# Performance work log

Hardware: AMD Instinct MI355X
Metric: run time of the kernel (lower is better)

The kernel has to match this reference:

```python
import jax, jax.numpy as jnp
import numpy as np

EPS = 1e-8  # torch cosine_similarity eps

def _cnorm(x):
    return jnp.maximum(jnp.linalg.norm(x, axis=-1), EPS)

def setup_inputs() -> dict:
    key = jax.random.key(0)
    ks = jax.random.split(key, 9)
    B, K, dp, Ms = 16384, 16, 64, 32
    content = jax.random.normal(ks[0], (B, K, dp), jnp.float32)
    types = jax.random.uniform(ks[1], (B, K, 3), jnp.float32)
    conf = jax.random.uniform(ks[2], (B, K), jnp.float32)
    S = jax.random.normal(ks[3], (B, Ms, dp), jnp.float32)
    s1 = 1.0 / np.sqrt(dp)   # torch Linear init bound, fan_in=dp
    s2 = 1.0 / np.sqrt(2 * dp)  # fan_in=2*dp
    W_ante = jax.random.uniform(ks[4], (dp, dp), jnp.float32, -s1, s1)
    W_cons = jax.random.uniform(ks[5], (dp, 2 * dp), jnp.float32, -s2, s2)
    W_gamma_w = jax.random.uniform(ks[6], (dp, 2 * dp), jnp.float32, -s2, s2)
    W_gamma_b = jnp.zeros((dp,), jnp.float32)
    log_fire_threshold = jnp.asarray(np.log(0.5), jnp.float32)
    return {"content": content, "types": types, "conf": conf, "S": S,
            "W_ante": W_ante, "W_cons": W_cons, "W_gamma_w": W_gamma_w,
            "W_gamma_b": W_gamma_b, "log_fire_threshold": log_fire_threshold}

def reference(content, types, conf, S, W_ante, W_cons, W_gamma_w, W_gamma_b, log_fire_threshold):
    # InferenceEngine.forward_chain, vectorized over rules and batch.
    B, K, dp = content.shape
    p_fact = types[..., 0]  # FACT channel
    p_rule = types[..., 1]  # RULE channel
    thr = jnp.exp(log_fire_threshold)

    ante = content @ W_ante.T                                   # [B,K,dp]
    dots = jnp.einsum('bkd,bjd->bkj', ante, content)            # [B,K_rule,K_fact]
    sim = dots / (_cnorm(ante)[:, :, None] * _cnorm(content)[:, None, :])
    match_scores = sim * p_fact[:, None, :]
    match_strength = jnp.einsum('bkj,bj->bk', match_scores, conf)
    fire = jax.nn.sigmoid((match_strength - thr) / 0.5) * p_rule  # [B,K]
    matched = jnp.einsum('bkj,bjd->bkd', match_scores, content)
    new_fact = jnp.concatenate([content, matched], -1) @ W_cons.T  # [B,K,dp]
    derived_conf = fire * conf                                     # [B,K]

    def soft_write(S, cand, dconf):
        # batched LatentScratchpad.soft_write; cand [B,dp], dconf [B]
        dot = jnp.einsum('bd,bmd->bm', cand, S)
        s = dot / (_cnorm(cand)[:, None] * _cnorm(S))
        alpha = jax.nn.softmax(s * 4.0, axis=-1)                  # [B,Ms]
        best = jnp.argmax(alpha, axis=-1)
        best_slots = jnp.take_along_axis(S, best[:, None, None], axis=1)[:, 0, :]
        gamma = jax.nn.sigmoid(jnp.concatenate([best_slots, cand], -1) @ W_gamma_w.T + W_gamma_b)
        new_content = gamma * cand + (1.0 - gamma) * best_slots
        return S + dconf[:, None, None] * alpha[..., None] * (new_content[:, None, :] - S)

    def step(S, xs):
        nf_k, fire_k, dc_k = xs
        S_w = soft_write(S, nf_k, dc_k)
        mask = (fire_k > 0.1)[:, None, None]  # replaces per-element .item() branch
        return jnp.where(mask, S_w, S), None

    xs = (jnp.swapaxes(new_fact, 0, 1), fire.T, derived_conf.T)   # scan over K rules (sequential dep on S)
    S_new, _ = jax.lax.scan(step, S, xs)
    best_derived_conf = jnp.max(derived_conf, axis=-1)
    return S_new, best_derived_conf
```

## Files before the change

### kernel.cpp

```cpp
#include <hip/hip_runtime.h>
#include <math.h>

typedef float v2f __attribute__((ext_vector_type(2)));
typedef float v4f __attribute__((ext_vector_type(4)));
typedef short bs8 __attribute__((ext_vector_type(8)));
typedef int   i4  __attribute__((ext_vector_type(4)));

__device__ __forceinline__ float hsum(v2f a) { return a.x + a.y; }
__device__ __forceinline__ float rsq_(float x) { return __builtin_amdgcn_rsqf(fmaxf(x, 1e-16f)); }
__device__ __forceinline__ float rcp_(float x) { return __builtin_amdgcn_rcpf(x); }

__device__ __forceinline__ void pk4(v2f& acc, v4f a, v4f b) {
    acc += a.xy * b.xy;
    acc += a.zw * b.zw;
}

__device__ __forceinline__ short bf16rne_(float x) {
    unsigned u = __float_as_uint(x);
    return (short)((u + 0x7FFFu + ((u >> 16) & 1)) >> 16);
}
__device__ __forceinline__ float bf2f_(short s) {
    return __uint_as_float((unsigned)(unsigned short)s << 16);
}
__device__ __forceinline__ int cvtpk_(float lo, float hi) {
    int r;
    asm("v_cvt_pk_bf16_f32 %0, %1, %2" : "=v"(r) : "v"(lo), "v"(hi));
    return r;
}
__device__ __forceinline__ float xsum32_(float x) {
    auto r = __builtin_amdgcn_permlane32_swap(__float_as_int(x), __float_as_int(x), false, false);
    return __int_as_float(r[0]) + __int_as_float(r[1]);
}

template<int CTRL>
__device__ __forceinline__ float dpp_add_(float x) {
    int r = __builtin_amdgcn_update_dpp(0, __float_as_int(x), CTRL, 0xF, 0xF, true);
    return x + __int_as_float(r);
}
template<int CTRL>
__device__ __forceinline__ float dpp_max_(float x) {
    int r = __builtin_amdgcn_update_dpp(__float_as_int(x), __float_as_int(x), CTRL, 0xF, 0xF, false);
    return fmaxf(x, __int_as_float(r));
}
__device__ __forceinline__ float dpp_sum32h(float x) {
    x = dpp_add_<0x111>(x);
    x = dpp_add_<0x112>(x);
    x = dpp_add_<0x114>(x);
    x = dpp_add_<0x118>(x);
    x = dpp_add_<0x142>(x);
    return __int_as_float(__builtin_amdgcn_readlane(__float_as_int(x), 31));
}
__device__ __forceinline__ float dpp_max32h(float x) {
    x = dpp_max_<0x111>(x);
    x = dpp_max_<0x112>(x);
    x = dpp_max_<0x114>(x);
    x = dpp_max_<0x118>(x);
    x = dpp_max_<0x142>(x);
    return __int_as_float(__builtin_amdgcn_readlane(__float_as_int(x), 31));
}

__global__ __launch_bounds__(256, 2)
void dense_kernel(const float* __restrict__ content,
                  const float* __restrict__ types,
                  const float* __restrict__ conf,
                  const float* __restrict__ W_ante,
                  const float* __restrict__ W_cons,
                  const float* __restrict__ W_gw,
                  const float* __restrict__ lft,
                  float* __restrict__ out, int B)
{
    const int tid = threadIdx.x;
    const int l = tid & 63;
    const int w = tid >> 6;
    const int b = blockIdx.x * 4 + w;

    __shared__ float s_cont[4][16*68];
    __shared__ float s_scr [4][16*68];
    __shared__ float s_ms  [4][16*20];
    __shared__ float s_sm  [4][96];
    __shared__ bs8   s_bA[512];
    __shared__ bs8   s_b1[512];
    __shared__ bs8   s_b2[512];
    __shared__ bs8   s_bG[512];

    #pragma unroll
    for (int it = 0; it < 8; it++) {
        const int fid = tid + it*256;
        const int mat = fid >> 9, rem = fid & 511;
        const int fl  = rem & 63;
        const int row = ((rem >> 7) & 3)*16 + (fl & 15);
        const int kb  = ((rem >> 6) & 1)*32 + (fl >> 4)*8;
        const float* src = (mat == 0) ? (W_ante + row*64 + kb)
                         : (mat == 1) ? (W_cons + row*128 + kb)
                         : (mat == 2) ? (W_cons + row*128 + 64 + kb)
                         :              (W_gw  + row*128 + 64 + kb);
        bs8 v;
        #pragma unroll
        for (int e = 0; e < 8; e++) v[e] = bf16rne_(src[e]);
        bs8* dst = (mat == 0) ? s_bA : (mat == 1) ? s_b1 : (mat == 2) ? s_b2 : s_bG;
        dst[rem] = v;
    }
    __syncthreads();
    if (b >= B) return;

    float* cont = s_cont[w];
    float* scr  = s_scr[w];
    float* ms   = s_ms[w];
    float* sm   = s_sm[w];

    const float thr = expf(lft[0]);

    float c[16];
    const float* cb = content + ((size_t)b << 10);
    #pragma unroll
    for (int k = 0; k < 16; k++) {
        float v = cb[(k << 6) + l];
        c[k] = v;
        cont[k*68 + l] = v;
    }
    if (l < 16) {
        sm[0  + l] = conf[((size_t)b << 4) + l];
        sm[16 + l] = types[(((size_t)b << 4) + l)*3 + 0];
        sm[32 + l] = types[(((size_t)b << 4) + l)*3 + 1];
    }

    {
        const int k = l & 15, q = l >> 4;
        const v4f* row = (const v4f*)&cont[k*68 + q*16];
        v2f s2 = {0.f, 0.f};
        #pragma unroll
        for (int i = 0; i < 4; i++) { v4f v = row[i]; pk4(s2, v, v); }
        float s = hsum(s2);
        s += __shfl_xor(s, 16, 64);
        s += __shfl_xor(s, 32, 64);
        if (l < 16) sm[48 + l] = rsq_(s);
    }

    bs8 aC[2];
    #pragma unroll
    for (int s = 0; s < 2; s++) {
        const float* ap = &cont[(l & 15)*68 + s*32 + (l >> 4)*8];
        v4f p0 = *(const v4f*)ap;
        v4f p1 = *(const v4f*)(ap + 4);
        bs8 v;
        v[0]=bf16rne_(p0.x); v[1]=bf16rne_(p0.y); v[2]=bf16rne_(p0.z); v[3]=bf16rne_(p0.w);
        v[4]=bf16rne_(p1.x); v[5]=bf16rne_(p1.y); v[6]=bf16rne_(p1.z); v[7]=bf16rne_(p1.w);
        aC[s] = v;
    }

    #pragma unroll
    for (int t = 0; t < 4; t++) {
        v4f acc = {0.f, 0.f, 0.f, 0.f};
        acc = __builtin_amdgcn_mfma_f32_16x16x32_bf16(aC[0], s_bA[(t*2+0)*64 + l], acc, 0, 0, 0);
        acc = __builtin_amdgcn_mfma_f32_16x16x32_bf16(aC[1], s_bA[(t*2+1)*64 + l], acc, 0, 0, 0);
        #pragma unroll
        for (int r = 0; r < 4; r++)
            scr[((l >> 4)*4 + r)*68 + t*16 + (l & 15)] = acc[r];
    }

    {
        const int k = l & 15, q = l >> 4;
        const v4f* row = (const v4f*)&scr[k*68 + q*16];
        v2f s2 = {0.f, 0.f};
        #pragma unroll
        for (int i = 0; i < 4; i++) { v4f v = row[i]; pk4(s2, v, v); }
        float s = hsum(s2);
        s += __shfl_xor(s, 16, 64);
        s += __shfl_xor(s, 32, 64);
        if (l < 16) sm[64 + l] = rsq_(s);
    }

    {
        const int k = l & 15, jg4 = (l >> 4) * 4;
        const v4f* ar = (const v4f*)&scr[k*68];
        const v4f* c0 = (const v4f*)&cont[(jg4+0)*68];
        const v4f* c1 = (const v4f*)&cont[(jg4+1)*68];
        const v4f* c2 = (const v4f*)&cont[(jg4+2)*68];
        const v4f* c3 = (const v4f*)&cont[(jg4+3)*68];
        v2f d0 = {0,0}, d1 = {0,0}, d2 = {0,0}, d3 = {0,0};
        #pragma unroll
        for (int i = 0; i < 16; i++) {
            v4f a = ar[i];
            v4f x0 = c0[i]; d0 += a.xy*x0.xy; d0 += a.zw*x0.zw;
            v4f x1 = c1[i]; d1 += a.xy*x1.xy; d1 += a.zw*x1.zw;
            v4f x2 = c2[i]; d2 += a.xy*x2.xy; d2 += a.zw*x2.zw;
            v4f x3 = c3[i]; d3 += a.xy*x3.xy; d3 += a.zw*x3.zw;
        }
        const float ra = sm[64 + k];
        v4f res;
        res.x = hsum(d0) * ra * sm[48 + jg4+0] * sm[16 + jg4+0];
        res.y = hsum(d1) * ra * sm[48 + jg4+1] * sm[16 + jg4+1];
        res.z = hsum(d2) * ra * sm[48 + jg4+2] * sm[16 + jg4+2];
        res.w = hsum(d3) * ra * sm[48 + jg4+3] * sm[16 + jg4+3];
        *(v4f*)&ms[k*20 + jg4] = res;
    }

    float dc_l = 0.f;
    if (l < 16) {
        const v4f* mr = (const v4f*)&ms[l*20];
        const v4f* cf = (const v4f*)&sm[0];
        v2f st = {0.f, 0.f};
        #pragma unroll
        for (int i = 0; i < 4; i++) { v4f m4 = mr[i]; v4f f4 = cf[i]; st += m4.xy*f4.xy; st += m4.zw*f4.zw; }
        float str = hsum(st);
        float fire = sm[32 + l] * rcp_(1.0f + __expf(-(str - thr) * 2.0f));
        float dcf  = fire * sm[0 + l];
        out[((size_t)b << 11) + 1024 + l] = fire;
        out[((size_t)b << 11) + 1040 + l] = dcf;
        dc_l = dcf;
    }
    {
        float mv = dc_l;
        mv = fmaxf(mv, __shfl_xor(mv, 1, 64));
        mv = fmaxf(mv, __shfl_xor(mv, 2, 64));
        mv = fmaxf(mv, __shfl_xor(mv, 4, 64));
        mv = fmaxf(mv, __shfl_xor(mv, 8, 64));
        if (l == 0) out[((size_t)B << 11) + b] = mv;
    }

    float mt[16];
    #pragma unroll
    for (int k = 0; k < 16; k++) {
        const v4f* mr = (const v4f*)&ms[k*20];
        v2f m2 = {0.f, 0.f};
        #pragma unroll
        for (int i = 0; i < 4; i++) {
            v4f m4 = mr[i];
            v2f clo = {c[4*i+0], c[4*i+1]};
            v2f chi = {c[4*i+2], c[4*i+3]};
            m2 += m4.xy*clo; m2 += m4.zw*chi;
        }
        mt[k] = hsum(m2);
    }
    #pragma unroll
    for (int k = 0; k < 16; k++) scr[k*68 + l] = mt[k];

    bs8 aM[2];
    #pragma unroll
    for (int s = 0; s < 2; s++) {
        const float* ap = &scr[(l & 15)*68 + s*32 + (l >> 4)*8];
        v4f p0 = *(const v4f*)ap;
        v4f p1 = *(const v4f*)(ap + 4);
        bs8 v;
        v[0]=bf16rne_(p0.x); v[1]=bf16rne_(p0.y); v[2]=bf16rne_(p0.z); v[3]=bf16rne_(p0.w);
        v[4]=bf16rne_(p1.x); v[5]=bf16rne_(p1.y); v[6]=bf16rne_(p1.z); v[7]=bf16rne_(p1.w);
        aM[s] = v;
    }

    v4f nfacc[4];
    #pragma unroll
    for (int t = 0; t < 4; t++) {
        v4f acc = {0.f, 0.f, 0.f, 0.f};
        acc = __builtin_amdgcn_mfma_f32_16x16x32_bf16(aC[0], s_b1[(t*2+0)*64 + l], acc, 0, 0, 0);
        acc = __builtin_amdgcn_mfma_f32_16x16x32_bf16(aC[1], s_b1[(t*2+1)*64 + l], acc, 0, 0, 0);
        acc = __builtin_amdgcn_mfma_f32_16x16x32_bf16(aM[0], s_b2[(t*2+0)*64 + l], acc, 0, 0, 0);
        acc = __builtin_amdgcn_mfma_f32_16x16x32_bf16(aM[1], s_b2[(t*2+1)*64 + l], acc, 0, 0, 0);
        nfacc[t] = acc;
    }

    #pragma unroll
    for (int t = 0; t < 4; t++) {
        #pragma unroll
        for (int r = 0; r < 4; r++) {
            const int krow = (l >> 4)*4 + r, dcol = t*16 + (l & 15);
            scr[krow*68 + dcol] = nfacc[t][r];
            out[((size_t)b << 11) + (size_t)(krow << 6) + dcol] = nfacc[t][r];
        }
    }

    #pragma unroll
    for (int r = 0; r < 4; r++) {
        float s = 0.f;
        #pragma unroll
        for (int t = 0; t < 4; t++) s += nfacc[t][r]*nfacc[t][r];
        s += __shfl_xor(s, 1, 64);
        s += __shfl_xor(s, 2, 64);
        s += __shfl_xor(s, 4, 64);
        s += __shfl_xor(s, 8, 64);
        if ((l & 15) == 0)
            out[((size_t)b << 11) + 1056 + (l >> 4)*4 + r] = rsq_(s);
    }

    bs8 aN[2];
    #pragma unroll
    for (int s = 0; s < 2; s++) {
        const float* ap = &scr[(l & 15)*68 + s*32 + (l >> 4)*8];
        v4f p0 = *(const v4f*)ap;
        v4f p1 = *(const v4f*)(ap + 4);
        bs8 v;
        v[0]=bf16rne_(p0.x); v[1]=bf16rne_(p0.y); v[2]=bf16rne_(p0.z); v[3]=bf16rne_(p0.w);
        v[4]=bf16rne_(p1.x); v[5]=bf16rne_(p1.y); v[6]=bf16rne_(p1.z); v[7]=bf16rne_(p1.w);
        aN[s] = v;
    }

    unsigned short* gco = (unsigned short*)(out + ((size_t)b << 11) + 1088);
    #pragma unroll
    for (int t = 0; t < 4; t++) {
        v4f acc = {0.f, 0.f, 0.f, 0.f};
        acc = __builtin_amdgcn_mfma_f32_16x16x32_bf16(aN[0], s_bG[(t*2+0)*64 + l], acc, 0, 0, 0);
        acc = __builtin_amdgcn_mfma_f32_16x16x32_bf16(aN[1], s_bG[(t*2+1)*64 + l], acc, 0, 0, 0);
        #pragma unroll
        for (int r = 0; r < 4; r++)
            gco[(((l >> 4)*4 + r) << 6) + t*16 + (l & 15)] = (unsigned short)bf16rne_(acc[r]);
    }
}

__global__ __launch_bounds__(512, 4)
void scan_kernel(const float* __restrict__ Sg,
                 const float* __restrict__ W_gw,
                 const float* __restrict__ W_gb,
                 float* __restrict__ out, int B)
{
    const int t = threadIdx.x;
    const int l = t & 63;
    const int w = t >> 6;
    const int b = (blockIdx.x << 3) + w;

    __shared__ bs8   bG2[512];
    __shared__ float snf_  [8][16*64];
    __shared__ float smeta_[8][48];
    __shared__ float bsb_  [8][68];
    float* snf   = snf_[w];
    float* smeta = smeta_[w];
    float* bsb   = bsb_[w];

    const int m = l & 31, h = l >> 5;

    {
        const int rem = t;
        const int fl  = rem & 63;
        const int row = ((rem >> 7) & 3)*16 + (fl & 15);
        const int kb  = ((rem >> 6) & 1)*32 + (fl >> 4)*8;
        const float* src = W_gw + (size_t)row*128 + kb;
        bs8 v;
        #pragma unroll
        for (int e = 0; e < 8; e++) v[e] = bf16rne_(src[e]);
        bG2[rem] = v;
    }

    v2f Sreg[16];

    if (b < B) {
        if (l < 48) smeta[l] = out[((size_t)b << 11) + 1024 + l];

        const float* nfb = out + ((size_t)b << 11);
        #pragma unroll
        for (int i = 0; i < 4; i++) {
            *(v4f*)&snf[i*256 + l*4] = *(const v4f*)&nfb[i*256 + l*4];
        }

        const float* srow = Sg + ((size_t)b << 11) + (m << 6) + (h << 5);
        #pragma unroll
        for (int i = 0; i < 8; i++) {
            v4f v = *(const v4f*)&srow[i*4];
            Sreg[2*i]   = v.xy;
            Sreg[2*i+1] = v.zw;
        }
    }

    __syncthreads();
    if (b >= B) return;

    const unsigned short* gcg = (const unsigned short*)(out + ((size_t)b << 11) + 1088);
    const float gb = W_gb[l];
    const int q = l >> 4;

    #pragma unroll 1
    for (int k = 0; k < 16; k++) {
        const float fire = smeta[k];
        if (fire <= 0.1f) continue;
        const float dck  = smeta[16 + k];
        const float rncn = smeta[32 + k];
        const unsigned short gcu = gcg[(k << 6) + l];
        const float cd   = snf[(k << 6) + l];

        v2f d2 = {0.f, 0.f}, n2 = {0.f, 0.f};
        {
            const v4f* cr = (const v4f*)&snf[(k << 6) + (h << 5)];
            #pragma unroll
            for (int i = 0; i < 8; i++) {
                v4f c = cr[i];
                d2 += Sreg[2*i]*c.xy;       d2 += Sreg[2*i+1]*c.zw;
                n2 += Sreg[2*i]*Sreg[2*i];  n2 += Sreg[2*i+1]*Sreg[2*i+1];
            }
        }
        const float dt = xsum32_(hsum(d2));
        const float nn = xsum32_(hsum(n2));
        const float sc = dt * rsq_(nn) * rncn;
        const float e  = __expf(4.0f * sc);

        const float mx = dpp_max32h(sc);
        const unsigned long long bal = __ballot(sc == mx);
        const int best = __ffsll(bal & 0xffffffffULL) - 1;

        if (m == best) {
            #pragma unroll
            for (int j = 0; j < 8; j++) {
                v4f v = { Sreg[2*j].x, Sreg[2*j].y, Sreg[2*j+1].x, Sreg[2*j+1].y };
                *(v4f*)&bsb[(h << 5) + j*4] = v;
            }
        }

        const float tot = dpp_sum32h(e);
        const float wm  = dck * e * rcp_(tot);

        bs8 af[2];
        #pragma unroll
        for (int s = 0; s < 2; s++) {
            const float* bp = &bsb[s*32 + q*8];
            v4f p0 = *(const v4f*)bp;
            v4f p1 = *(const v4f*)(bp + 4);
            i4 pk;
            pk[0] = cvtpk_(p0.x, p0.y);
            pk[1] = cvtpk_(p0.z, p0.w);
            pk[2] = cvtpk_(p1.x, p1.y);
            pk[3] = cvtpk_(p1.z, p1.w);
            af[s] = __builtin_bit_cast(bs8, pk);
        }
        __builtin_amdgcn_s_setprio(1);
        v4f g0 = {0,0,0,0}, g1 = {0,0,0,0}, g2a = {0,0,0,0}, g3 = {0,0,0,0};
        g0 = __builtin_amdgcn_mfma_f32_16x16x32_bf16(af[0], bG2[0*64 + l], g0, 0, 0, 0);
        g1 = __builtin_amdgcn_mfma_f32_16x16x32_bf16(af[0], bG2[2*64 + l], g1, 0, 0, 0);
        g2a = __builtin_amdgcn_mfma_f32_16x16x32_bf16(af[0], bG2[4*64 + l], g2a, 0, 0, 0);
        g3 = __builtin_amdgcn_mfma_f32_16x16x32_bf16(af[0], bG2[6*64 + l], g3, 0, 0, 0);
        g0 = __builtin_amdgcn_mfma_f32_16x16x32_bf16(af[1], bG2[1*64 + l], g0, 0, 0, 0);
        g1 = __builtin_amdgcn_mfma_f32_16x16x32_bf16(af[1], bG2[3*64 + l], g1, 0, 0, 0);
        g2a = __builtin_amdgcn_mfma_f32_16x16x32_bf16(af[1], bG2[5*64 + l], g2a, 0, 0, 0);
        g3 = __builtin_amdgcn_mfma_f32_16x16x32_bf16(af[1], bG2[7*64 + l], g3, 0, 0, 0);
        __builtin_amdgcn_s_setprio(0);
        const float gdot = (q < 2) ? ((q == 0) ? g0[0] : g1[0])
                                   : ((q == 2) ? g2a[0] : g3[0]);

        const float gck = bf2f_((short)gcu);
        const float g = gb + gck + gdot;
        const float gamma = rcp_(1.0f + __expf(-g));
        const float bsd = bsb[l];
        bsb[l] = gamma*cd + (1.0f - gamma)*bsd;

        const v2f wm2 = {wm, wm};
        {
            const v4f* nr = (const v4f*)&bsb[h << 5];
            #pragma unroll
            for (int i = 0; i < 8; i++) {
                v4f nc = nr[i];
                Sreg[2*i]   += wm2 * (nc.xy - Sreg[2*i]);
                Sreg[2*i+1] += wm2 * (nc.zw - Sreg[2*i+1]);
            }
        }
    }

    {
        float* ob = out + ((size_t)b << 11) + (m << 6) + (h << 5);
        #pragma unroll
        for (int j = 0; j < 8; j++) {
            v4f v = { Sreg[2*j].x, Sreg[2*j].y, Sreg[2*j+1].x, Sreg[2*j+1].y };
            *(v4f*)&ob[j*4] = v;
        }
    }
}

extern "C" void kernel_launch(void* const* d_in, const int* in_sizes, int n_in,
                              void* d_out, int out_size, void* d_ws, size_t ws_size,
                              hipStream_t stream) {
    const float* content = (const float*)d_in[0];
    const float* types   = (const float*)d_in[1];
    const float* conf    = (const float*)d_in[2];
    const float* S       = (const float*)d_in[3];
    const float* W_ante  = (const float*)d_in[4];
    const float* W_cons  = (const float*)d_in[5];
    const float* W_gw    = (const float*)d_in[6];
    const float* W_gb    = (const float*)d_in[7];
    const float* lft     = (const float*)d_in[8];

    const int B = in_sizes[0] / 1024;

    hipLaunchKernelGGL(dense_kernel, dim3((B + 3) / 4), dim3(256), 0, stream,
                       content, types, conf, W_ante, W_cons, W_gw, lft, (float*)d_out, B);
    hipLaunchKernelGGL(scan_kernel, dim3((B + 7) / 8), dim3(512), 0, stream,
                       S, W_gw, W_gb, (float*)d_out, B);
}
```

Measured before the change: 199.2 us.

## Fuse dense and scan kernels, keeping intermediates in shared memory

```diff
diff --git a/kernel.cpp b/kernel.cpp
--- a/kernel.cpp
+++ b/kernel.cpp
@@ -22,8 +22,8 @@
 __device__ __forceinline__ float bf2f_(short s) {
     return __uint_as_float((unsigned)(unsigned short)s << 16);
 }
-__device__ __forceinline__ int cvtpk_(float lo, float hi) {
-    int r;
+__device__ __forceinline__ unsigned cvtpk_(float lo, float hi) {
+    unsigned r;
     asm("v_cvt_pk_bf16_f32 %0, %1, %2" : "=v"(r) : "v"(lo), "v"(hi));
     return r;
 }
@@ -60,12 +60,14 @@
 }
 
 __global__ __launch_bounds__(256, 2)
-void dense_kernel(const float* __restrict__ content,
+void fused_kernel(const float* __restrict__ content,
                   const float* __restrict__ types,
                   const float* __restrict__ conf,
+                  const float* __restrict__ Sg,
                   const float* __restrict__ W_ante,
                   const float* __restrict__ W_cons,
                   const float* __restrict__ W_gw,
+                  const float* __restrict__ W_gb,
                   const float* __restrict__ lft,
                   float* __restrict__ out, int B)
 {
@@ -73,6 +75,7 @@
     const int l = tid & 63;
     const int w = tid >> 6;
     const int b = blockIdx.x * 4 + w;
+    const bool act = (b < B);
 
     __shared__ float s_cont[4][16*68];
     __shared__ float s_scr [4][16*68];
@@ -82,6 +85,14 @@
     __shared__ bs8   s_b1[512];
     __shared__ bs8   s_b2[512];
     __shared__ bs8   s_bG[512];
+
+    float* cont = s_cont[w];
+    float* scr  = s_scr[w];
+    float* ms   = s_ms[w];
+    float* sm   = s_sm[w];
+    unsigned short* gcB = (unsigned short*)cont;
+    float* smeta = cont + 512;
+    float* bsb   = cont + 560;
 
     #pragma unroll
     for (int it = 0; it < 8; it++) {
@@ -101,233 +112,217 @@
         dst[rem] = v;
     }
     __syncthreads();
-    if (b >= B) return;
-
-    float* cont = s_cont[w];
-    float* scr  = s_scr[w];
-    float* ms   = s_ms[w];
-    float* sm   = s_sm[w];
 
     const float thr = expf(lft[0]);
 
-    float c[16];
-    const float* cb = content + ((size_t)b << 10);
+    if (act) {
+        float c[16];
+        const float* cb = content + ((size_t)b << 10);
+        #pragma unroll
+        for (int k = 0; k < 16; k++) {
+            float v = cb[(k << 6) + l];
+            c[k] = v;
+            cont[k*68 + l] = v;
+        }
+        if (l < 16) {
+            sm[0  + l] = conf[((size_t)b << 4) + l];
+            sm[16 + l] = types[(((size_t)b << 4) + l)*3 + 0];
+            sm[32 + l] = types[(((size_t)b << 4) + l)*3 + 1];
+        }
+
+        {
+            const int k = l & 15, q = l >> 4;
+            const v4f* row = (const v4f*)&cont[k*68 + q*16];
+            v2f s2 = {0.f, 0.f};
+            #pragma unroll
+            for (int i = 0; i < 4; i++) { v4f v = row[i]; pk4(s2, v, v); }
+            float s = hsum(s2);
+            s += __shfl_xor(s, 16, 64);
+            s += __shfl_xor(s, 32, 64);
+            if (l < 16) sm[48 + l] = rsq_(s);
+        }
+
+        bs8 aC[2];
+        #pragma unroll
+        for (int s = 0; s < 2; s++) {
+            const float* ap = &cont[(l & 15)*68 + s*32 + (l >> 4)*8];
+            v4f p0 = *(const v4f*)ap;
+            v4f p1 = *(const v4f*)(ap + 4);
+            bs8 v;
+            v[0]=bf16rne_(p0.x); v[1]=bf16rne_(p0.y); v[2]=bf16rne_(p0.z); v[3]=bf16rne_(p0.w);
+            v[4]=bf16rne_(p1.x); v[5]=bf16rne_(p1.y); v[6]=bf16rne_(p1.z); v[7]=bf16rne_(p1.w);
+            aC[s] = v;
+        }
+
+        #pragma unroll
+        for (int t = 0; t < 4; t++) {
+            v4f acc = {0.f, 0.f, 0.f, 0.f};
+            acc = __builtin_amdgcn_mfma_f32_16x16x32_bf16(aC[0], s_bA[(t*2+0)*64 + l], acc, 0, 0, 0);
+            acc = __builtin_amdgcn_mfma_f32_16x16x32_bf16(aC[1], s_bA[(t*2+1)*64 + l], acc, 0, 0, 0);
+            #pragma unroll
+            for (int r = 0; r < 4; r++)
+                scr[((l >> 4)*4 + r)*68 + t*16 + (l & 15)] = acc[r];
+        }
+
+        {
+            const int k = l & 15, q = l >> 4;
+            const v4f* row = (const v4f*)&scr[k*68 + q*16];
+            v2f s2 = {0.f, 0.f};
+            #pragma unroll
+            for (int i = 0; i < 4; i++) { v4f v = row[i]; pk4(s2, v, v); }
+            float s = hsum(s2);
+            s += __shfl_xor(s, 16, 64);
+            s += __shfl_xor(s, 32, 64);
+            if (l < 16) sm[64 + l] = rsq_(s);
+        }
+
+        {
+            const int k = l & 15, jg4 = (l >> 4) * 4;
+            const v4f* ar = (const v4f*)&scr[k*68];
+            const v4f* c0 = (const v4f*)&cont[(jg4+0)*68];
+            const v4f* c1 = (const v4f*)&cont[(jg4+1)*68];
+            const v4f* c2 = (const v4f*)&cont[(jg4+2)*68];
+            const v4f* c3 = (const v4f*)&cont[(jg4+3)*68];
+            v2f d0 = {0,0}, d1 = {0,0}, d2 = {0,0}, d3 = {0,0};
+            #pragma unroll
+            for (int i = 0; i < 16; i++) {
+                v4f a = ar[i];
+                v4f x0 = c0[i]; d0 += a.xy*x0.xy; d0 += a.zw*x0.zw;
+                v4f x1 = c1[i]; d1 += a.xy*x1.xy; d1 += a.zw*x1.zw;
+                v4f x2 = c2[i]; d2 += a.xy*x2.xy; d2 += a.zw*x2.zw;
+                v4f x3 = c3[i]; d3 += a.xy*x3.xy; d3 += a.zw*x3.zw;
+            }
+            const float ra = sm[64 + k];
+            v4f res;
+            res.x = hsum(d0) * ra * sm[48 + jg4+0] * sm[16 + jg4+0];
+            res.y = hsum(d1) * ra * sm[48 + jg4+1] * sm[16 + jg4+1];
+            res.z = hsum(d2) * ra * sm[48 + jg4+2] * sm[16 + jg4+2];
+            res.w = hsum(d3) * ra * sm[48 + jg4+3] * sm[16 + jg4+3];
+            *(v4f*)&ms[k*20 + jg4] = res;
+        }
+
+        float dc_l = 0.f;
+        if (l < 16) {
+            const v4f* mr = (const v4f*)&ms[l*20];
+            const v4f* cf = (const v4f*)&sm[0];
+            v2f st = {0.f, 0.f};
+            #pragma unroll
+            for (int i = 0; i < 4; i++) { v4f m4 = mr[i]; v4f f4 = cf[i]; st += m4.xy*f4.xy; st += m4.zw*f4.zw; }
+            float str = hsum(st);
+            float fire = sm[32 + l] * rcp_(1.0f + __expf(-(str - thr) * 2.0f));
+            float dcf  = fire * sm[0 + l];
+            smeta[l]      = fire;
+            smeta[16 + l] = dcf;
+            dc_l = dcf;
+        }
+        {
+            float mv = dc_l;
+            mv = fmaxf(mv, __shfl_xor(mv, 1, 64));
+            mv = fmaxf(mv, __shfl_xor(mv, 2, 64));
+            mv = fmaxf(mv, __shfl_xor(mv, 4, 64));
+            mv = fmaxf(mv, __shfl_xor(mv, 8, 64));
+            if (l == 0) out[((size_t)B << 11) + b] = mv;
+        }
+
+        float mt[16];
+        #pragma unroll
+        for (int k = 0; k < 16; k++) {
+            const v4f* mr = (const v4f*)&ms[k*20];
+            v2f m2 = {0.f, 0.f};
+            #pragma unroll
+            for (int i = 0; i < 4; i++) {
+                v4f m4 = mr[i];
+                v2f clo = {c[4*i+0], c[4*i+1]};
+                v2f chi = {c[4*i+2], c[4*i+3]};
+                m2 += m4.xy*clo; m2 += m4.zw*chi;
+            }
+            mt[k] = hsum(m2);
+        }
+        #pragma unroll
+        for (int k = 0; k < 16; k++) scr[k*68 + l] = mt[k];
+
+        bs8 aM[2];
+        #pragma unroll
+        for (int s = 0; s < 2; s++) {
+            const float* ap = &scr[(l & 15)*68 + s*32 + (l >> 4)*8];
+            v4f p0 = *(const v4f*)ap;
+            v4f p1 = *(const v4f*)(ap + 4);
+            bs8 v;
+            v[0]=bf16rne_(p0.x); v[1]=bf16rne_(p0.y); v[2]=bf16rne_(p0.z); v[3]=bf16rne_(p0.w);
+            v[4]=bf16rne_(p1.x); v[5]=bf16rne_(p1.y); v[6]=bf16rne_(p1.z); v[7]=bf16rne_(p1.w);
+            aM[s] = v;
+        }
+
+        v4f nfacc[4];
+        #pragma unroll
+        for (int t = 0; t < 4; t++) {
+            v4f acc = {0.f, 0.f, 0.f, 0.f};
+            acc = __builtin_amdgcn_mfma_f32_16x16x32_bf16(aC[0], s_b1[(t*2+0)*64 + l], acc, 0, 0, 0);
+            acc = __builtin_amdgcn_mfma_f32_16x16x32_bf16(aC[1], s_b1[(t*2+1)*64 + l], acc, 0, 0, 0);
+            acc = __builtin_amdgcn_mfma_f32_16x16x32_bf16(aM[0], s_b2[(t*2+0)*64 + l], acc, 0, 0, 0);
+            acc = __builtin_amdgcn_mfma_f32_16x16x32_bf16(aM[1], s_b2[(t*2+1)*64 + l], acc, 0, 0, 0);
+            nfacc[t] = acc;
+        }
+
+        #pragma unroll
+        for (int t = 0; t < 4; t++) {
+            #pragma unroll
+            for (int r = 0; r < 4; r++)
+                scr[((l >> 4)*4 + r)*68 + t*16 + (l & 15)] = nfacc[t][r];
+        }
+
+        #pragma unroll
+        for (int r = 0; r < 4; r++) {
+            float s = 0.f;
+            #pragma unroll
+            for (int t = 0; t < 4; t++) s += nfacc[t][r]*nfacc[t][r];
+            s += __shfl_xor(s, 1, 64);
+            s += __shfl_xor(s, 2, 64);
+            s += __shfl_xor(s, 4, 64);
+            s += __shfl_xor(s, 8, 64);
+            if ((l & 15) == 0)
+                smeta[32 + (l >> 4)*4 + r] = rsq_(s);
+        }
+
+        bs8 aN[2];
+        #pragma unroll
+        for (int s = 0; s < 2; s++) {
+            const float* ap = &scr[(l & 15)*68 + s*32 + (l >> 4)*8];
+            v4f p0 = *(const v4f*)ap;
+            v4f p1 = *(const v4f*)(ap + 4);
+            bs8 v;
+            v[0]=bf16rne_(p0.x); v[1]=bf16rne_(p0.y); v[2]=bf16rne_(p0.z); v[3]=bf16rne_(p0.w);
+            v[4]=bf16rne_(p1.x); v[5]=bf16rne_(p1.y); v[6]=bf16rne_(p1.z); v[7]=bf16rne_(p1.w);
+            aN[s] = v;
+        }
+
+        #pragma unroll
+        for (int t = 0; t < 4; t++) {
+            v4f acc = {0.f, 0.f, 0.f, 0.f};
+            acc = __builtin_amdgcn_mfma_f32_16x16x32_bf16(aN[0], s_bG[(t*2+0)*64 + l], acc, 0, 0, 0);
+            acc = __builtin_amdgcn_mfma_f32_16x16x32_bf16(aN[1], s_bG[(t*2+1)*64 + l], acc, 0, 0, 0);
+            #pragma unroll
+            for (int r = 0; r < 4; r++)
+                gcB[(((l >> 4)*4 + r) << 6) + t*16 + (l & 15)] = (unsigned short)bf16rne_(acc[r]);
+        }
+    }
+
+    const int m = l & 31, h = l >> 5;
+    v2f Sreg[16];
+    if (act) {
+        const float* srow = Sg + ((size_t)b << 11) + (m << 6) + (h << 5);
+        #pragma unroll
+        for (int i = 0; i < 8; i++) {
+            v4f v = *(const v4f*)&srow[i*4];
+            Sreg[2*i]   = v.xy;
+            Sreg[2*i+1] = v.zw;
+        }
+    }
+
+    __syncthreads();
     #pragma unroll
-    for (int k = 0; k < 16; k++) {
-        float v = cb[(k << 6) + l];
-        c[k] = v;
-        cont[k*68 + l] = v;
-    }
-    if (l < 16) {
-        sm[0  + l] = conf[((size_t)b << 4) + l];
-        sm[16 + l] = types[(((size_t)b << 4) + l)*3 + 0];
-        sm[32 + l] = types[(((size_t)b << 4) + l)*3 + 1];
-    }
-
-    {
-        const int k = l & 15, q = l >> 4;
-        const v4f* row = (const v4f*)&cont[k*68 + q*16];
-        v2f s2 = {0.f, 0.f};
-        #pragma unroll
-        for (int i = 0; i < 4; i++) { v4f v = row[i]; pk4(s2, v, v); }
-        float s = hsum(s2);
-        s += __shfl_xor(s, 16, 64);
-        s += __shfl_xor(s, 32, 64);
-        if (l < 16) sm[48 + l] = rsq_(s);
-    }
-
-    bs8 aC[2];
-    #pragma unroll
-    for (int s = 0; s < 2; s++) {
-        const float* ap = &cont[(l & 15)*68 + s*32 + (l >> 4)*8];
-        v4f p0 = *(const v4f*)ap;
-        v4f p1 = *(const v4f*)(ap + 4);
-        bs8 v;
-        v[0]=bf16rne_(p0.x); v[1]=bf16rne_(p0.y); v[2]=bf16rne_(p0.z); v[3]=bf16rne_(p0.w);
-        v[4]=bf16rne_(p1.x); v[5]=bf16rne_(p1.y); v[6]=bf16rne_(p1.z); v[7]=bf16rne_(p1.w);
-        aC[s] = v;
-    }
-
-    #pragma unroll
-    for (int t = 0; t < 4; t++) {
-        v4f acc = {0.f, 0.f, 0.f, 0.f};
-        acc = __builtin_amdgcn_mfma_f32_16x16x32_bf16(aC[0], s_bA[(t*2+0)*64 + l], acc, 0, 0, 0);
-        acc = __builtin_amdgcn_mfma_f32_16x16x32_bf16(aC[1], s_bA[(t*2+1)*64 + l], acc, 0, 0, 0);
-        #pragma unroll
-        for (int r = 0; r < 4; r++)
-            scr[((l >> 4)*4 + r)*68 + t*16 + (l & 15)] = acc[r];
-    }
-
-    {
-        const int k = l & 15, q = l >> 4;
-        const v4f* row = (const v4f*)&scr[k*68 + q*16];
-        v2f s2 = {0.f, 0.f};
-        #pragma unroll
-        for (int i = 0; i < 4; i++) { v4f v = row[i]; pk4(s2, v, v); }
-        float s = hsum(s2);
-        s += __shfl_xor(s, 16, 64);
-        s += __shfl_xor(s, 32, 64);
-        if (l < 16) sm[64 + l] = rsq_(s);
-    }
-
-    {
-        const int k = l & 15, jg4 = (l >> 4) * 4;
-        const v4f* ar = (const v4f*)&scr[k*68];
-        const v4f* c0 = (const v4f*)&cont[(jg4+0)*68];
-        const v4f* c1 = (const v4f*)&cont[(jg4+1)*68];
-        const v4f* c2 = (const v4f*)&cont[(jg4+2)*68];
-        const v4f* c3 = (const v4f*)&cont[(jg4+3)*68];
-        v2f d0 = {0,0}, d1 = {0,0}, d2 = {0,0}, d3 = {0,0};
-        #pragma unroll
-        for (int i = 0; i < 16; i++) {
-            v4f a = ar[i];
-            v4f x0 = c0[i]; d0 += a.xy*x0.xy; d0 += a.zw*x0.zw;
-            v4f x1 = c1[i]; d1 += a.xy*x1.xy; d1 += a.zw*x1.zw;
-            v4f x2 = c2[i]; d2 += a.xy*x2.xy; d2 += a.zw*x2.zw;
-            v4f x3 = c3[i]; d3 += a.xy*x3.xy; d3 += a.zw*x3.zw;
-        }
-        const float ra = sm[64 + k];
-        v4f res;
-        res.x = hsum(d0) * ra * sm[48 + jg4+0] * sm[16 + jg4+0];
-        res.y = hsum(d1) * ra * sm[48 + jg4+1] * sm[16 + jg4+1];
-        res.z = hsum(d2) * ra * sm[48 + jg4+2] * sm[16 + jg4+2];
-        res.w = hsum(d3) * ra * sm[48 + jg4+3] * sm[16 + jg4+3];
-        *(v4f*)&ms[k*20 + jg4] = res;
-    }
-
-    float dc_l = 0.f;
-    if (l < 16) {
-        const v4f* mr = (const v4f*)&ms[l*20];
-        const v4f* cf = (const v4f*)&sm[0];
-        v2f st = {0.f, 0.f};
-        #pragma unroll
-        for (int i = 0; i < 4; i++) { v4f m4 = mr[i]; v4f f4 = cf[i]; st += m4.xy*f4.xy; st += m4.zw*f4.zw; }
-        float str = hsum(st);
-        float fire = sm[32 + l] * rcp_(1.0f + __expf(-(str - thr) * 2.0f));
-        float dcf  = fire * sm[0 + l];
-        out[((size_t)b << 11) + 1024 + l] = fire;
-        out[((size_t)b << 11) + 1040 + l] = dcf;
-        dc_l = dcf;
-    }
-    {
-        float mv = dc_l;
-        mv = fmaxf(mv, __shfl_xor(mv, 1, 64));
-        mv = fmaxf(mv, __shfl_xor(mv, 2, 64));
-        mv = fmaxf(mv, __shfl_xor(mv, 4, 64));
-        mv = fmaxf(mv, __shfl_xor(mv, 8, 64));
-        if (l == 0) out[((size_t)B << 11) + b] = mv;
-    }
-
-    float mt[16];
-    #pragma unroll
-    for (int k = 0; k < 16; k++) {
-        const v4f* mr = (const v4f*)&ms[k*20];
-        v2f m2 = {0.f, 0.f};
-        #pragma unroll
-        for (int i = 0; i < 4; i++) {
-            v4f m4 = mr[i];
-            v2f clo = {c[4*i+0], c[4*i+1]};
-            v2f chi = {c[4*i+2], c[4*i+3]};
-            m2 += m4.xy*clo; m2 += m4.zw*chi;
-        }
-        mt[k] = hsum(m2);
-    }
-    #pragma unroll
-    for (int k = 0; k < 16; k++) scr[k*68 + l] = mt[k];
-
-    bs8 aM[2];
-    #pragma unroll
-    for (int s = 0; s < 2; s++) {
-        const float* ap = &scr[(l & 15)*68 + s*32 + (l >> 4)*8];
-        v4f p0 = *(const v4f*)ap;
-        v4f p1 = *(const v4f*)(ap + 4);
-        bs8 v;
-        v[0]=bf16rne_(p0.x); v[1]=bf16rne_(p0.y); v[2]=bf16rne_(p0.z); v[3]=bf16rne_(p0.w);
-        v[4]=bf16rne_(p1.x); v[5]=bf16rne_(p1.y); v[6]=bf16rne_(p1.z); v[7]=bf16rne_(p1.w);
-        aM[s] = v;
-    }
-
-    v4f nfacc[4];
-    #pragma unroll
-    for (int t = 0; t < 4; t++) {
-        v4f acc = {0.f, 0.f, 0.f, 0.f};
-        acc = __builtin_amdgcn_mfma_f32_16x16x32_bf16(aC[0], s_b1[(t*2+0)*64 + l], acc, 0, 0, 0);
-        acc = __builtin_amdgcn_mfma_f32_16x16x32_bf16(aC[1], s_b1[(t*2+1)*64 + l], acc, 0, 0, 0);
-        acc = __builtin_amdgcn_mfma_f32_16x16x32_bf16(aM[0], s_b2[(t*2+0)*64 + l], acc, 0, 0, 0);
-        acc = __builtin_amdgcn_mfma_f32_16x16x32_bf16(aM[1], s_b2[(t*2+1)*64 + l], acc, 0, 0, 0);
-        nfacc[t] = acc;
-    }
-
-    #pragma unroll
-    for (int t = 0; t < 4; t++) {
-        #pragma unroll
-        for (int r = 0; r < 4; r++) {
-            const int krow = (l >> 4)*4 + r, dcol = t*16 + (l & 15);
-            scr[krow*68 + dcol] = nfacc[t][r];
-            out[((size_t)b << 11) + (size_t)(krow << 6) + dcol] = nfacc[t][r];
-        }
-    }
-
-    #pragma unroll
-    for (int r = 0; r < 4; r++) {
-        float s = 0.f;
-        #pragma unroll
-        for (int t = 0; t < 4; t++) s += nfacc[t][r]*nfacc[t][r];
-        s += __shfl_xor(s, 1, 64);
-        s += __shfl_xor(s, 2, 64);
-        s += __shfl_xor(s, 4, 64);
-        s += __shfl_xor(s, 8, 64);
-        if ((l & 15) == 0)
-            out[((size_t)b << 11) + 1056 + (l >> 4)*4 + r] = rsq_(s);
-    }
-
-    bs8 aN[2];
-    #pragma unroll
-    for (int s = 0; s < 2; s++) {
-        const float* ap = &scr[(l & 15)*68 + s*32 + (l >> 4)*8];
-        v4f p0 = *(const v4f*)ap;
-        v4f p1 = *(const v4f*)(ap + 4);
-        bs8 v;
-        v[0]=bf16rne_(p0.x); v[1]=bf16rne_(p0.y); v[2]=bf16rne_(p0.z); v[3]=bf16rne_(p0.w);
-        v[4]=bf16rne_(p1.x); v[5]=bf16rne_(p1.y); v[6]=bf16rne_(p1.z); v[7]=bf16rne_(p1.w);
-        aN[s] = v;
-    }
-
-    unsigned short* gco = (unsigned short*)(out + ((size_t)b << 11) + 1088);
-    #pragma unroll
-    for (int t = 0; t < 4; t++) {
-        v4f acc = {0.f, 0.f, 0.f, 0.f};
-        acc = __builtin_amdgcn_mfma_f32_16x16x32_bf16(aN[0], s_bG[(t*2+0)*64 + l], acc, 0, 0, 0);
-        acc = __builtin_amdgcn_mfma_f32_16x16x32_bf16(aN[1], s_bG[(t*2+1)*64 + l], acc, 0, 0, 0);
-        #pragma unroll
-        for (int r = 0; r < 4; r++)
-            gco[(((l >> 4)*4 + r) << 6) + t*16 + (l & 15)] = (unsigned short)bf16rne_(acc[r]);
-    }
-}
-
-__global__ __launch_bounds__(512, 4)
-void scan_kernel(const float* __restrict__ Sg,
-                 const float* __restrict__ W_gw,
-                 const float* __restrict__ W_gb,
-                 float* __restrict__ out, int B)
-{
-    const int t = threadIdx.x;
-    const int l = t & 63;
-    const int w = t >> 6;
-    const int b = (blockIdx.x << 3) + w;
-
-    __shared__ bs8   bG2[512];
-    __shared__ float snf_  [8][16*64];
-    __shared__ float smeta_[8][48];
-    __shared__ float bsb_  [8][68];
-    float* snf   = snf_[w];
-    float* smeta = smeta_[w];
-    float* bsb   = bsb_[w];
-
-    const int m = l & 31, h = l >> 5;
-
-    {
-        const int rem = t;
+    for (int j = 0; j < 2; j++) {
+        const int rem = tid + j*256;
         const int fl  = rem & 63;
         const int row = ((rem >> 7) & 3)*16 + (fl & 15);
         const int kb  = ((rem >> 6) & 1)*32 + (fl >> 4)*8;
@@ -335,33 +330,11 @@
         bs8 v;
         #pragma unroll
         for (int e = 0; e < 8; e++) v[e] = bf16rne_(src[e]);
-        bG2[rem] = v;
-    }
-
-    v2f Sreg[16];
-
-    if (b < B) {
-        if (l < 48) smeta[l] = out[((size_t)b << 11) + 1024 + l];
-
-        const float* nfb = out + ((size_t)b << 11);
-        #pragma unroll
-        for (int i = 0; i < 4; i++) {
-            *(v4f*)&snf[i*256 + l*4] = *(const v4f*)&nfb[i*256 + l*4];
-        }
-
-        const float* srow = Sg + ((size_t)b << 11) + (m << 6) + (h << 5);
-        #pragma unroll
-        for (int i = 0; i < 8; i++) {
-            v4f v = *(const v4f*)&srow[i*4];
-            Sreg[2*i]   = v.xy;
-            Sreg[2*i+1] = v.zw;
-        }
-    }
-
+        s_bA[rem] = v;
+    }
     __syncthreads();
-    if (b >= B) return;
-
-    const unsigned short* gcg = (const unsigned short*)(out + ((size_t)b << 11) + 1088);
+    if (!act) return;
+
     const float gb = W_gb[l];
     const int q = l >> 4;
 
@@ -371,12 +344,12 @@
         if (fire <= 0.1f) continue;
         const float dck  = smeta[16 + k];
         const float rncn = smeta[32 + k];
-        const unsigned short gcu = gcg[(k << 6) + l];
-        const float cd   = snf[(k << 6) + l];
+        const unsigned short gcu = gcB[(k << 6) + l];
+        const float cd   = scr[k*68 + l];
 
         v2f d2 = {0.f, 0.f}, n2 = {0.f, 0.f};
         {
-            const v4f* cr = (const v4f*)&snf[(k << 6) + (h << 5)];
+            const v4f* cr = (const v4f*)&scr[k*68 + (h << 5)];
             #pragma unroll
             for (int i = 0; i < 8; i++) {
                 v4f c = cr[i];
@@ -411,22 +384,22 @@
             v4f p0 = *(const v4f*)bp;
             v4f p1 = *(const v4f*)(bp + 4);
             i4 pk;
-            pk[0] = cvtpk_(p0.x, p0.y);
-            pk[1] = cvtpk_(p0.z, p0.w);
-            pk[2] = cvtpk_(p1.x, p1.y);
-            pk[3] = cvtpk_(p1.z, p1.w);
+            pk[0] = (int)cvtpk_(p0.x, p0.y);
+            pk[1] = (int)cvtpk_(p0.z, p0.w);
+            pk[2] = (int)cvtpk_(p1.x, p1.y);
+            pk[3] = (int)cvtpk_(p1.z, p1.w);
             af[s] = __builtin_bit_cast(bs8, pk);
         }
         __builtin_amdgcn_s_setprio(1);
         v4f g0 = {0,0,0,0}, g1 = {0,0,0,0}, g2a = {0,0,0,0}, g3 = {0,0,0,0};
-        g0 = __builtin_amdgcn_mfma_f32_16x16x32_bf16(af[0], bG2[0*64 + l], g0, 0, 0, 0);
-        g1 = __builtin_amdgcn_mfma_f32_16x16x32_bf16(af[0], bG2[2*64 + l], g1, 0, 0, 0);
-        g2a = __builtin_amdgcn_mfma_f32_16x16x32_bf16(af[0], bG2[4*64 + l], g2a, 0, 0, 0);
-        g3 = __builtin_amdgcn_mfma_f32_16x16x32_bf16(af[0], bG2[6*64 + l], g3, 0, 0, 0);
-        g0 = __builtin_amdgcn_mfma_f32_16x16x32_bf16(af[1], bG2[1*64 + l], g0, 0, 0, 0);
-        g1 = __builtin_amdgcn_mfma_f32_16x16x32_bf16(af[1], bG2[3*64 + l], g1, 0, 0, 0);
-        g2a = __builtin_amdgcn_mfma_f32_16x16x32_bf16(af[1], bG2[5*64 + l], g2a, 0, 0, 0);
-        g3 = __builtin_amdgcn_mfma_f32_16x16x32_bf16(af[1], bG2[7*64 + l], g3, 0, 0, 0);
+        g0 = __builtin_amdgcn_mfma_f32_16x16x32_bf16(af[0], s_bA[0*64 + l], g0, 0, 0, 0);
+        g1 = __builtin_amdgcn_mfma_f32_16x16x32_bf16(af[0], s_bA[2*64 + l], g1, 0, 0, 0);
+        g2a = __builtin_amdgcn_mfma_f32_16x16x32_bf16(af[0], s_bA[4*64 + l], g2a, 0, 0, 0);
+        g3 = __builtin_amdgcn_mfma_f32_16x16x32_bf16(af[0], s_bA[6*64 + l], g3, 0, 0, 0);
+        g0 = __builtin_amdgcn_mfma_f32_16x16x32_bf16(af[1], s_bA[1*64 + l], g0, 0, 0, 0);
+        g1 = __builtin_amdgcn_mfma_f32_16x16x32_bf16(af[1], s_bA[3*64 + l], g1, 0, 0, 0);
+        g2a = __builtin_amdgcn_mfma_f32_16x16x32_bf16(af[1], s_bA[5*64 + l], g2a, 0, 0, 0);
+        g3 = __builtin_amdgcn_mfma_f32_16x16x32_bf16(af[1], s_bA[7*64 + l], g3, 0, 0, 0);
         __builtin_amdgcn_s_setprio(0);
         const float gdot = (q < 2) ? ((q == 0) ? g0[0] : g1[0])
                                    : ((q == 2) ? g2a[0] : g3[0]);
@@ -474,8 +447,7 @@
 
     const int B = in_sizes[0] / 1024;
 
-    hipLaunchKernelGGL(dense_kernel, dim3((B + 3) / 4), dim3(256), 0, stream,
-                       content, types, conf, W_ante, W_cons, W_gw, lft, (float*)d_out, B);
-    hipLaunchKernelGGL(scan_kernel, dim3((B + 7) / 8), dim3(512), 0, stream,
-                       S, W_gw, W_gb, (float*)d_out, B);
-}
+    hipLaunchKernelGGL(fused_kernel, dim3((B + 3) / 4), dim3(256), 0, stream,
+                       content, types, conf, S, W_ante, W_cons, W_gw, W_gb, lft,
+                       (float*)d_out, B);
+}
```

Result: slower. 218.3 us (+9.6%).
